# Performance work log

Hardware: AMD Instinct MI355X
Metric: run time of the kernel (lower is better)

## Reference

```python
import jax, jax.numpy as jnp
import numpy as np

B, L, H, R = 4, 192, 768, 24


def setup_inputs() -> dict:
    key = jax.random.key(0)
    ks = jax.random.split(key, 18)
    s = 0.02
    inp = {
        "embed_tokens": jax.random.normal(ks[0], (B, L, H), dtype=jnp.float32),
        "attention_mask": jnp.ones((B, L), dtype=jnp.int32),
        "target_rel": jax.random.randint(ks[1], (B,), 0, R),
        # hidden_relational: Linear(H, H//2) stored as [in, out]
        "W_relh": jax.random.normal(ks[2], (H, H // 2), dtype=jnp.float32) * s,
        "b_relh": jnp.zeros((H // 2,), dtype=jnp.float32),
        # rel_judge: Linear(H//2, R)
        "W_rj": jax.random.normal(ks[3], (H // 2, R), dtype=jnp.float32) * s,
        "b_rj": jnp.zeros((R,), dtype=jnp.float32),
        # hidden_corres: Linear(2H, H)
        "W_corr": jax.random.normal(ks[4], (2 * H, H), dtype=jnp.float32) * s,
        "b_corr": jnp.zeros((H,), dtype=jnp.float32),
        # global_corr: Linear(H, 1)
        "W_gc": jax.random.normal(ks[5], (H, 1), dtype=jnp.float32) * s,
        "b_gc": jnp.zeros((1,), dtype=jnp.float32),
        # rel_embedding: Embedding(R, H)
        "rel_emb": jax.random.normal(ks[6], (R, H), dtype=jnp.float32) * s,
        # hidden_tag: Linear(2H, H) (fusion_type='concat' => multiplier 2)
        "W_tag": jax.random.normal(ks[7], (2 * H, H), dtype=jnp.float32) * s,
        "b_tag": jnp.zeros((H,), dtype=jnp.float32),
        # tag_subject / tag_object: Linear(H, 3)
        "W_sub": jax.random.normal(ks[8], (H, 3), dtype=jnp.float32) * s,
        "b_sub": jnp.zeros((3,), dtype=jnp.float32),
        "W_obj": jax.random.normal(ks[9], (H, 3), dtype=jnp.float32) * s,
        "b_obj": jnp.zeros((3,), dtype=jnp.float32),
    }
    return inp


def reference(embed_tokens, attention_mask, target_rel,
              W_relh, b_relh, W_rj, b_rj,
              W_corr, b_corr, W_gc, b_gc,
              rel_emb, W_tag, b_tag,
              W_sub, b_sub, W_obj, b_obj):
    # mode == 'train' path of PRGC.forward, with embed_tokens standing in for
    # bert(...)['last_hidden_state'].
    mask = attention_mask.astype(embed_tokens.dtype)  # [B,L]
    # stage 1: masked average pool -> relation judgement
    avg = jnp.sum(embed_tokens * mask[:, :, None], axis=1) / jnp.sum(mask, axis=1)[:, None]  # [B,H]
    rel_hidden = jax.nn.relu(avg @ W_relh + b_relh)
    stage1 = rel_hidden @ W_rj + b_rj  # [B,R]

    # correspondence matrix. concat_matrix[b,i,j] = [embed[b,j], embed[b,i]]
    # Linear on a concat is separable: split W_corr into the halves acting on
    # each operand, compute two [B,L,H] projections, sum with broadcasting.
    Hd = W_corr.shape[0] // 2
    h_first = embed_tokens @ W_corr[:Hd]   # acts on embed[b,j]
    h_second = embed_tokens @ W_corr[Hd:]  # acts on embed[b,i]
    corres_hidden = jax.nn.relu(h_first[:, None, :, :] + h_second[:, :, None, :] + b_corr)  # [B,L,L,H]
    pred_corres = corres_hidden @ W_gc + b_gc  # [B,L,L,1]

    # stage 2 tagging (train mode: gather gold relation embeddings)
    rel_e = rel_emb[target_rel]  # [B,H]
    rel_e = jnp.broadcast_to(rel_e[:, None, :], embed_tokens.shape)  # [B,L,H]
    fusion = jnp.concatenate([rel_e, embed_tokens], axis=-1) @ W_tag + b_tag  # [B,L,H] (no activation, as in source)
    subj_pred_tag = fusion @ W_sub + b_sub  # [B,L,3]
    obj_pred_tag = fusion @ W_obj + b_obj   # [B,L,3]
    return (stage1, subj_pred_tag, obj_pred_tag, pred_corres)
```

## Files before the change

kernel.cpp:

```cpp
#include <hip/hip_runtime.h>

#define H   768
#define Hh  384
#define LL  192
#define RR  24
#define HH  589824

typedef __attribute__((ext_vector_type(8))) short bf16x8;
typedef __attribute__((ext_vector_type(4))) float f32x4;

__device__ __forceinline__ unsigned short f2bf(float f) {
    unsigned int u = __float_as_uint(f);
    return (unsigned short)((u + 0x7FFF + ((u >> 16) & 1)) >> 16);
}

__device__ __forceinline__ void gload16(const void* g, void* l) {
    __builtin_amdgcn_global_load_lds(
        (const __attribute__((address_space(1))) unsigned int*)g,
        (__attribute__((address_space(3))) unsigned int*)l, 16, 0, 0);
}

__device__ __forceinline__ float wred(float v) {
#pragma unroll
    for (int off = 1; off < 64; off <<= 1) v += __shfl_xor(v, off);
    return v;
}

__global__ __launch_bounds__(256) void k_pre(
    const float* __restrict__ emb, const int* __restrict__ mask,
    const float* __restrict__ W_corr, const float* __restrict__ W_tag,
    const float* __restrict__ W_gc, const float* __restrict__ b_corr,
    const float* __restrict__ W_sub, const float* __restrict__ b_sub,
    const float* __restrict__ W_obj, const float* __restrict__ b_obj,
    const float* __restrict__ b_tag,
    float* __restrict__ avg_ws, unsigned short* __restrict__ embh,
    unsigned short* __restrict__ wct0, unsigned short* __restrict__ wct1,
    float* __restrict__ W8_ws, float* __restrict__ V8_ws,
    float* __restrict__ cb_ws, float* __restrict__ bc_ws)
{
    const int bid = blockIdx.x, tid = threadIdx.x;

    if (bid < 24) {
        __shared__ float msk[LL];
        __shared__ float part[32];
        __shared__ float msumS;
        __shared__ float4 red4[8][32];
        const int b  = bid / 6;
        const int h0 = (bid % 6) * 128;
        const int tx = tid & 31, ty = tid >> 5;
        if (tid < LL) msk[tid] = (float)mask[b * LL + tid];
        __syncthreads();
        if (tid < 32) {
            float s = 0.f;
            for (int k = tid; k < LL; k += 32) s += msk[k];
            part[tid] = s;
        }
        __syncthreads();
        if (tid == 0) {
            float s = 0.f;
            for (int k = 0; k < 32; ++k) s += part[k];
            msumS = s;
        }
        float4 acc = make_float4(0.f, 0.f, 0.f, 0.f);
        for (int l = ty; l < LL; l += 8) {
            const size_t o = (size_t)(b * LL + l) * H + h0 + tx * 4;
            const float m = msk[l];
            const float4 v = *(const float4*)(emb + o);
            acc.x += v.x * m; acc.y += v.y * m; acc.z += v.z * m; acc.w += v.w * m;
            ushort4 pk;
            pk.x = f2bf(v.x); pk.y = f2bf(v.y); pk.z = f2bf(v.z); pk.w = f2bf(v.w);
            *(ushort4*)(embh + o) = pk;
        }
        red4[ty][tx] = acc;
        __syncthreads();
        if (tid < 32) {
            float4 s = red4[0][tid];
#pragma unroll
            for (int r = 1; r < 8; ++r) {
                s.x += red4[r][tid].x; s.y += red4[r][tid].y;
                s.z += red4[r][tid].z; s.w += red4[r][tid].w;
            }
            const float inv = 1.f / msumS;
            s.x *= inv; s.y *= inv; s.z *= inv; s.w *= inv;
            *(float4*)(avg_ws + (size_t)b * H + h0 + tid * 4) = s;
        }
        return;
    }

    if (bid < 600) {
        const int local = bid - 24;
        const int m  = local / 288;
        const int r2 = local % 288;
        const int ko = r2 / 3, nb = r2 % 3;
        const int n  = nb * 256 + tid;
        const float* src = (m == 0) ? W_corr : W_corr + HH;
        unsigned short* dst = (m == 0) ? wct0 : wct1;
        union { unsigned short u[8]; uint4 v; } pk;
#pragma unroll
        for (int q = 0; q < 8; ++q)
            pk.u[q] = f2bf(src[(size_t)(ko * 8 + q) * H + n]);
        *(uint4*)(dst + (size_t)n * H + ko * 8) = pk.v;
        return;
    }

    if (bid < 792) {
        const int wave = tid >> 6, lane = tid & 63;
        const int k = (bid - 600) * 4 + wave;
        const float* rc0 = W_corr + (size_t)k * H;
        const float* rc1 = W_corr + (size_t)HH + (size_t)k * H;
        const float* rtl = W_tag + (size_t)k * H;
        const float* rth = W_tag + (size_t)(H + k) * H;
        float u0 = 0.f, u1 = 0.f;
        float wsv[3] = {0, 0, 0}, wov[3] = {0, 0, 0};
        float vsv[3] = {0, 0, 0}, vov[3] = {0, 0, 0};
#pragma unroll
        for (int it = 0; it < 3; ++it) {
            const int h = lane * 4 + it * 256;
            const float4 c0 = *(const float4*)(rc0 + h);
            const float4 c1 = *(const float4*)(rc1 + h);
            const float4 tl = *(const float4*)(rtl + h);
            const float4 th = *(const float4*)(rth + h);
            const float4 g  = *(const float4*)(W_gc + h);
            float su[12], ob[12];
            *(float4*)&su[0] = *(const float4*)(W_sub + h * 3);
            *(float4*)&su[4] = *(const float4*)(W_sub + h * 3 + 4);
            *(float4*)&su[8] = *(const float4*)(W_sub + h * 3 + 8);
            *(float4*)&ob[0] = *(const float4*)(W_obj + h * 3);
            *(float4*)&ob[4] = *(const float4*)(W_obj + h * 3 + 4);
            *(float4*)&ob[8] = *(const float4*)(W_obj + h * 3 + 8);
            u0 += c0.x * g.x + c0.y * g.y + c0.z * g.z + c0.w * g.w;
            u1 += c1.x * g.x + c1.y * g.y + c1.z * g.z + c1.w * g.w;
            const float t4[4] = {th.x, th.y, th.z, th.w};
            const float l4[4] = {tl.x, tl.y, tl.z, tl.w};
#pragma unroll
            for (int d = 0; d < 4; ++d)
#pragma unroll
                for (int c = 0; c < 3; ++c) {
                    wsv[c] += t4[d] * su[d * 3 + c];
                    vsv[c] += l4[d] * su[d * 3 + c];
                    wov[c] += t4[d] * ob[d * 3 + c];
                    vov[c] += l4[d] * ob[d * 3 + c];
                }
        }
        u0 = wred(u0); u1 = wred(u1);
#pragma unroll
        for (int c = 0; c < 3; ++c) {
            wsv[c] = wred(wsv[c]); wov[c] = wred(wov[c]);
            vsv[c] = wred(vsv[c]); vov[c] = wred(vov[c]);
        }
        if (lane == 0) {
            *(float4*)(W8_ws + k * 8)     = make_float4(u0, u1, wsv[0], wsv[1]);
            *(float4*)(W8_ws + k * 8 + 4) = make_float4(wsv[2], wov[0], wov[1], wov[2]);
            *(float4*)(V8_ws + k * 8)     = make_float4(vsv[0], vsv[1], vsv[2], vov[0]);
            *(float4*)(V8_ws + k * 8 + 4) = make_float4(vov[1], vov[2], 0.f, 0.f);
        }
        return;
    }

    {
        const int wave = tid >> 6, lane = tid & 63;
        if (wave == 0) {
            float cs[3] = {0, 0, 0}, co[3] = {0, 0, 0};
#pragma unroll
            for (int it = 0; it < 3; ++it) {
                const int h = lane * 4 + it * 256;
                const float4 bt = *(const float4*)(b_tag + h);
                float su[12], ob[12];
                *(float4*)&su[0] = *(const float4*)(W_sub + h * 3);
                *(float4*)&su[4] = *(const float4*)(W_sub + h * 3 + 4);
                *(float4*)&su[8] = *(const float4*)(W_sub + h * 3 + 8);
                *(float4*)&ob[0] = *(const float4*)(W_obj + h * 3);
                *(float4*)&ob[4] = *(const float4*)(W_obj + h * 3 + 4);
                *(float4*)&ob[8] = *(const float4*)(W_obj + h * 3 + 8);
                const float b4[4] = {bt.x, bt.y, bt.z, bt.w};
#pragma unroll
                for (int d = 0; d < 4; ++d)
#pragma unroll
                    for (int c = 0; c < 3; ++c) {
                        cs[c] += b4[d] * su[d * 3 + c];
                        co[c] += b4[d] * ob[d * 3 + c];
                    }
            }
#pragma unroll
            for (int c = 0; c < 3; ++c) { cs[c] = wred(cs[c]); co[c] = wred(co[c]); }
            if (lane == 0) {
#pragma unroll
                for (int c = 0; c < 3; ++c) {
                    cb_ws[c]     = cs[c] + b_sub[c];
                    cb_ws[3 + c] = co[c] + b_obj[c];
                }
            }
        } else if (wave == 1) {
            float s = 0.f;
#pragma unroll
            for (int it = 0; it < 3; ++it) {
                const int h = lane * 4 + it * 256;
                const float4 bcv = *(const float4*)(b_corr + h);
                const float4 g   = *(const float4*)(W_gc + h);
                s += bcv.x * g.x + bcv.y * g.y + bcv.z * g.z + bcv.w * g.w;
            }
            s = wred(s);
            if (lane == 0) bc_ws[0] = s;
        }
    }
}

__global__ __launch_bounds__(256) void k_main(
    const unsigned short* __restrict__ embh, const unsigned short* __restrict__ wct0,
    const unsigned short* __restrict__ wct1, const float* __restrict__ b_corr,
    const float* __restrict__ W_relh, const float* __restrict__ avg_ws,
    const int* __restrict__ target_rel, const float* __restrict__ rel_emb,
    const float* __restrict__ V8_ws, const float* __restrict__ cb_ws,
    float* __restrict__ hfb, float* __restrict__ hsb,
    float* __restrict__ relh_part, float* __restrict__ tb_ws)
{
    __shared__ unsigned short As[2][4096];
    __shared__ unsigned short Bs[2][4096];
    const int bid = blockIdx.x, tid = threadIdx.x;

    if (bid >= 288) {
        if (bid < 480) {
            float* red = (float*)&As[0][0];
            const int rb = bid - 288;
            const int kc = rb & 7;
            const int t2 = rb >> 3;
            const int b  = t2 / 6;
            const int o0 = (t2 % 6) * 64;
            const int tx = tid & 63, ty = tid >> 6;
            const int h0 = kc * 96 + ty * 24;
            float s = 0.f;
            for (int h = h0; h < h0 + 24; ++h)
                s += avg_ws[(size_t)b * H + h] * W_relh[(size_t)h * Hh + o0 + tx];
            red[ty * 64 + tx] = s;
            __syncthreads();
            if (ty == 0)
                relh_part[(size_t)(kc * 4 + b) * Hh + o0 + tx] =
                    red[tx] + red[64 + tx] + red[128 + tx] + red[192 + tx];
        } else {
            const int b = tid >> 6, lane = tid & 63;
            const float* re = rel_emb + (size_t)target_rel[b] * H;
            float t[6] = {0, 0, 0, 0, 0, 0};
#pragma unroll
            for (int it = 0; it < 12; ++it) {
                const int k = lane + it * 64;
                const float rl = re[k];
                const float4 a = *(const float4*)(V8_ws + k * 8);
                const float4 v = *(const float4*)(V8_ws + k * 8 + 4);
                t[0] += rl * a.x; t[1] += rl * a.y; t[2] += rl * a.z;
                t[3] += rl * a.w; t[4] += rl * v.x; t[5] += rl * v.y;
            }
#pragma unroll
            for (int c = 0; c < 6; ++c) t[c] = wred(t[c]);
            if (lane == 0) {
#pragma unroll
                for (int c = 0; c < 6; ++c)
                    tb_ws[b * 8 + c] = t[c] + cb_ws[c];
            }
        }
        return;
    }

    const int sel = bid / 144;
    const int tt  = bid % 144;
    const int mt = tt % 12, nt = tt / 12;
    const int m0 = mt * 64, n0 = nt * 64;
    const unsigned short* Bsrc = sel ? wct1 : wct0;
    float* C = sel ? hsb : hfb;

    const int wv = tid >> 6, ln = tid & 63;
    const int lr = ln & 15, ko = ln >> 4;
    const int wr = (wv >> 1) * 32, wc = (wv & 1) * 32;

    f32x4 acc[2][2];
#pragma unroll
    for (int mi = 0; mi < 2; ++mi)
#pragma unroll
        for (int ni = 0; ni < 2; ++ni)
            acc[mi][ni] = (f32x4){0.f, 0.f, 0.f, 0.f};

    auto stage = [&](int buf, int k0) {
#pragma unroll
        for (int it = 0; it < 2; ++it) {
            const int sbase = it * 256 + wv * 64;
            const int slot = sbase + ln;
            const int r = slot >> 3, c = slot & 7;
            const int cs = c ^ (r & 7);
            gload16(embh + (size_t)(m0 + r) * H + k0 + cs * 8, &As[buf][sbase * 8]);
            gload16(Bsrc + (size_t)(n0 + r) * H + k0 + cs * 8, &Bs[buf][sbase * 8]);
        }
    };

    stage(0, 0);
    int cur = 0;
    for (int ks = 0; ks < 12; ++ks) {
        __syncthreads();
        if (ks < 11) stage(cur ^ 1, (ks + 1) * 64);
        bf16x8 af[2][2], bfr[2][2];
#pragma unroll
        for (int mi = 0; mi < 2; ++mi) {
            const int r = wr + mi * 16 + lr;
#pragma unroll
            for (int kc = 0; kc < 2; ++kc) {
                const int qs = (kc * 4 + ko) ^ (r & 7);
                af[kc][mi] = *(const bf16x8*)(&As[cur][r * 64 + qs * 8]);
            }
        }
#pragma unroll
        for (int ni = 0; ni < 2; ++ni) {
            const int r = wc + ni * 16 + lr;
#pragma unroll
            for (int kc = 0; kc < 2; ++kc) {
                const int qs = (kc * 4 + ko) ^ (r & 7);
                bfr[kc][ni] = *(const bf16x8*)(&Bs[cur][r * 64 + qs * 8]);
            }
        }
#pragma unroll
        for (int kc = 0; kc < 2; ++kc)
#pragma unroll
            for (int mi = 0; mi < 2; ++mi)
#pragma unroll
                for (int ni = 0; ni < 2; ++ni)
                    acc[mi][ni] = __builtin_amdgcn_mfma_f32_16x16x32_bf16(
                        af[kc][mi], bfr[kc][ni], acc[mi][ni], 0, 0, 0);
        cur ^= 1;
    }

    float cbv[2];
#pragma unroll
    for (int ni = 0; ni < 2; ++ni)
        cbv[ni] = (sel == 0) ? b_corr[n0 + wc + ni * 16 + lr] : 0.f;
#pragma unroll
    for (int mi = 0; mi < 2; ++mi)
#pragma unroll
        for (int ni = 0; ni < 2; ++ni) {
            const int m = m0 + wr + mi * 16 + ko * 4;
            const int n = n0 + wc + ni * 16 + lr;
#pragma unroll
            for (int rr = 0; rr < 4; ++rr)
                C[(size_t)(m + rr) * H + n] = acc[mi][ni][rr] + cbv[ni];
        }
}

__global__ __launch_bounds__(256) void k_tail(
    const float* __restrict__ hfb, const float* __restrict__ hsb,
    const float* __restrict__ emb, const float* __restrict__ W8_ws,
    const float* __restrict__ tb_ws, const float* __restrict__ relh_part,
    const float* __restrict__ b_relh, const float* __restrict__ W_gc,
    const float* __restrict__ W_rj, const float* __restrict__ b_rj,
    float* __restrict__ cpart, float* __restrict__ hfw_ws,
    float* __restrict__ out)
{
    __shared__ float hfT[96][34];
    const int bid = blockIdx.x, tid = threadIdx.x;

    if (bid < 576) {
        const int s    = bid & 7;
        const int tile = bid >> 3;
        const int b   = tile / 18;
        const int rem = tile % 18;
        const int i0  = (rem / 6) * 64;
        const int j0  = (rem % 6) * 32;
        const int h0  = s * 96;
        const int tx = tid & 15, ty = tid >> 4;

#pragma unroll
        for (int it = 0; it < 3; ++it) {
            const int j = tid >> 3, q = tid & 7;
            const int k = it * 32 + q * 4;
            const float4 fv = *(const float4*)(hfb + (size_t)(b * LL + j0 + j) * H + h0 + k);
            hfT[k + 0][j] = fv.x;
            hfT[k + 1][j] = fv.y;
            hfT[k + 2][j] = fv.z;
            hfT[k + 3][j] = fv.w;
        }
        __syncthreads();

        float acc[4][2] = {{0.f}};
        float hsr[4][8];
        const float* hsbase = hsb + (size_t)(b * LL + i0 + ty * 4) * H + h0;

        for (int kb = 0; kb < 96; kb += 8) {
#pragma unroll
            for (int ii = 0; ii < 4; ++ii) {
                const float4 v0 = *(const float4*)(hsbase + (size_t)ii * H + kb);
                const float4 v1 = *(const float4*)(hsbase + (size_t)ii * H + kb + 4);
                hsr[ii][0] = v0.x; hsr[ii][1] = v0.y; hsr[ii][2] = v0.z; hsr[ii][3] = v0.w;
                hsr[ii][4] = v1.x; hsr[ii][5] = v1.y; hsr[ii][6] = v1.z; hsr[ii][7] = v1.w;
            }
            const float4 wa = *(const float4*)(W_gc + h0 + kb);
            const float4 wb = *(const float4*)(W_gc + h0 + kb + 4);
            const float wreg[8] = {wa.x, wa.y, wa.z, wa.w, wb.x, wb.y, wb.z, wb.w};
#pragma unroll
            for (int k8 = 0; k8 < 8; ++k8) {
                const int kk = kb + k8;
                const float2 f2 = *(const float2*)&hfT[kk][tx * 2];
                const float w = wreg[k8];
#pragma unroll
                for (int ii = 0; ii < 4; ++ii) {
                    acc[ii][0] += fabsf(f2.x + hsr[ii][k8]) * w;
                    acc[ii][1] += fabsf(f2.y + hsr[ii][k8]) * w;
                }
            }
        }
#pragma unroll
        for (int ii = 0; ii < 4; ++ii) {
            *(float2*)(cpart + (size_t)s * 147456 + (size_t)b * 36864
                       + (size_t)(i0 + ty * 4 + ii) * LL + j0 + tx * 2) =
                make_float2(acc[ii][0], acc[ii][1]);
        }
    } else if (bid < 768) {
        const int wave = tid >> 6, lane = tid & 63;
        const int r = (bid - 576) * 4 + wave;
        const int b = r / LL;
        const float* er = emb + (size_t)r * H;
        float s0 = 0.f, s1 = 0.f;
        float t[6] = {0, 0, 0, 0, 0, 0};
#pragma unroll
        for (int it = 0; it < 12; ++it) {
            const int h = lane + it * 64;
            const float e = er[h];
            const float4 a = *(const float4*)(W8_ws + h * 8);
            const float4 v = *(const float4*)(W8_ws + h * 8 + 4);
            s0 += e * a.x; s1 += e * a.y;
            t[0] += e * a.z; t[1] += e * a.w; t[2] += e * v.x;
            t[3] += e * v.y; t[4] += e * v.z; t[5] += e * v.w;
        }
        s0 = wred(s0); s1 = wred(s1);
#pragma unroll
        for (int c = 0; c < 6; ++c) t[c] = wred(t[c]);
        if (lane == 0) {
            hfw_ws[r] = s0;
            hfw_ws[768 + r] = s1;
#pragma unroll
            for (int c = 0; c < 3; ++c) {
                out[96 + r * 3 + c]   = t[c]     + tb_ws[b * 8 + c];
                out[2400 + r * 3 + c] = t[3 + c] + tb_ws[b * 8 + 3 + c];
            }
        }
    } else {
        float* relhS = &hfT[0][0];
        for (int i = tid; i < 4 * Hh; i += 256) {
            const int b = i / Hh, o = i % Hh;
            float s = b_relh[o];
#pragma unroll
            for (int kc = 0; kc < 8; ++kc)
                s += relh_part[(size_t)(kc * 4 + b) * Hh + o];
            relhS[i] = fmaxf(s, 0.f);
        }
        __syncthreads();
        if (tid < 96) {
            const int b = tid / RR, rj = tid % RR;
            float s = b_rj[rj];
            for (int k = 0; k < Hh; ++k)
                s += relhS[b * Hh + k] * W_rj[k * RR + rj];
            out[b * RR + rj] = s;
        }
    }
}

__global__ __launch_bounds__(256) void k_merge(
    const float* __restrict__ cpart, const float* __restrict__ hfw_ws,
    const float* __restrict__ bc_ws, const float* __restrict__ b_gc,
    float* __restrict__ out)
{
    const int idx = blockIdx.x * 256 + threadIdx.x;
    const int b  = idx / 9216;
    const int rr = idx % 9216;
    const int i  = rr / 48;
    const int j4 = (rr % 48) * 4;
    const size_t off = (size_t)b * 36864 + (size_t)i * LL + j4;

    float4 p = make_float4(0.f, 0.f, 0.f, 0.f);
#pragma unroll
    for (int s = 0; s < 8; ++s) {
        const float4 v = *(const float4*)(cpart + (size_t)s * 147456 + off);
        p.x += v.x; p.y += v.y; p.z += v.z; p.w += v.w;
    }
    const float4 hw = *(const float4*)(hfw_ws + b * LL + j4);
    const float hs = hfw_ws[768 + b * LL + i];
    const float bc = bc_ws[0];
    const float bg = b_gc[0];

    float4 o;
    o.x = 0.5f * (p.x + hw.x + hs + bc) + bg;
    o.y = 0.5f * (p.y + hw.y + hs + bc) + bg;
    o.z = 0.5f * (p.z + hw.z + hs + bc) + bg;
    o.w = 0.5f * (p.w + hw.w + hs + bc) + bg;
    *(float4*)(out + 4704 + off) = o;
}

extern "C" void kernel_launch(void* const* d_in, const int* in_sizes, int n_in,
                              void* d_out, int out_size, void* d_ws, size_t ws_size,
                              hipStream_t stream) {
    const float* emb    = (const float*)d_in[0];
    const int*   mask   = (const int*)d_in[1];
    const int*   trel   = (const int*)d_in[2];
    const float* W_relh = (const float*)d_in[3];
    const float* b_relh = (const float*)d_in[4];
    const float* W_rj   = (const float*)d_in[5];
    const float* b_rj   = (const float*)d_in[6];
    const float* W_corr = (const float*)d_in[7];
    const float* b_corr = (const float*)d_in[8];
    const float* W_gc   = (const float*)d_in[9];
    const float* b_gc   = (const float*)d_in[10];
    const float* relemb = (const float*)d_in[11];
    const float* W_tag  = (const float*)d_in[12];
    const float* b_tag  = (const float*)d_in[13];
    const float* W_sub  = (const float*)d_in[14];
    const float* b_sub  = (const float*)d_in[15];
    const float* W_obj  = (const float*)d_in[16];
    const float* b_obj  = (const float*)d_in[17];

    float* out = (float*)d_out;
    float* ws  = (float*)d_ws;
    float* hfb  = ws;
    float* hsb  = ws + (size_t)HH;
    unsigned short* embh = (unsigned short*)(ws + (size_t)2 * HH);
    unsigned short* wct0 = embh + (size_t)HH;
    unsigned short* wct1 = wct0 + (size_t)HH;
    float* smalls    = ws + (size_t)2 * HH + (size_t)3 * HH / 2;
    float* avg_ws    = smalls;
    float* W8_ws     = avg_ws + 4 * H;
    float* V8_ws     = W8_ws + 8 * H;
    float* relh_part = V8_ws + 8 * H;
    float* hfw_ws    = relh_part + 32 * Hh;
    float* tb_ws     = hfw_ws + 1536;
    float* cb_ws     = tb_ws + 32;
    float* bc_ws     = cb_ws + 8;
    float* cpart     = bc_ws + 8 + 200;

    k_pre<<<793, 256, 0, stream>>>(emb, mask, W_corr, W_tag, W_gc, b_corr,
                                   W_sub, b_sub, W_obj, b_obj, b_tag,
                                   avg_ws, embh, wct0, wct1,
                                   W8_ws, V8_ws, cb_ws, bc_ws);
    k_main<<<481, 256, 0, stream>>>(embh, wct0, wct1, b_corr,
                                    W_relh, avg_ws, trel, relemb,
                                    V8_ws, cb_ws,
                                    hfb, hsb, relh_part, tb_ws);
    k_tail<<<769, 256, 0, stream>>>(hfb, hsb, emb, W8_ws, tb_ws,
                                    relh_part, b_relh, W_gc, W_rj, b_rj,
                                    cpart, hfw_ws, out);
    k_merge<<<144, 256, 0, stream>>>(cpart, hfw_ws, bc_ws, b_gc, out);
}
```

Before: 52.91 us.

## Fuse prep into GEMM kernel, convert fp32 to bf16 on load, merge tail stages

Drops the separate pre-pass that converted embeddings and W_corr to bf16 workspaces. The GEMM blocks now load fp32 operands through registers, convert them to bf16 and write them to LDS with register double-buffering. The masked-average and relation-hidden partials, the weight folding and the bias work become side blocks in the same launch. The tag-bias reduction moves into the second kernel, and the merge, tag output and stage-1 head are combined into a third kernel, going from four launches to three. This removes one launch and the bf16 round trip through global memory, at the cost of fp32 global reads and conversion work inside the GEMM main loop, plus a per-block redundant average recompute.

```diff
diff --git a/kernel.cpp b/kernel.cpp
--- a/kernel.cpp
+++ b/kernel.cpp
@@ -14,157 +14,90 @@
     return (unsigned short)((u + 0x7FFF + ((u >> 16) & 1)) >> 16);
 }
 
-__device__ __forceinline__ void gload16(const void* g, void* l) {
-    __builtin_amdgcn_global_load_lds(
-        (const __attribute__((address_space(1))) unsigned int*)g,
-        (__attribute__((address_space(3))) unsigned int*)l, 16, 0, 0);
-}
-
 __device__ __forceinline__ float wred(float v) {
 #pragma unroll
     for (int off = 1; off < 64; off <<= 1) v += __shfl_xor(v, off);
     return v;
 }
 
-__global__ __launch_bounds__(256) void k_pre(
+__global__ __launch_bounds__(256) void k_A(
     const float* __restrict__ emb, const int* __restrict__ mask,
     const float* __restrict__ W_corr, const float* __restrict__ W_tag,
-    const float* __restrict__ W_gc, const float* __restrict__ b_corr,
+    const float* __restrict__ W_gc, const float* __restrict__ W_relh,
     const float* __restrict__ W_sub, const float* __restrict__ b_sub,
     const float* __restrict__ W_obj, const float* __restrict__ b_obj,
-    const float* __restrict__ b_tag,
-    float* __restrict__ avg_ws, unsigned short* __restrict__ embh,
-    unsigned short* __restrict__ wct0, unsigned short* __restrict__ wct1,
+    const float* __restrict__ b_tag, const float* __restrict__ b_corr,
+    float* __restrict__ hfb, float* __restrict__ hsb,
+    float* __restrict__ relh_part,
     float* __restrict__ W8_ws, float* __restrict__ V8_ws,
     float* __restrict__ cb_ws, float* __restrict__ bc_ws)
 {
+    __shared__ unsigned short As[2][4096];
+    __shared__ unsigned short Bs[2][4096];
     const int bid = blockIdx.x, tid = threadIdx.x;
 
-    if (bid < 24) {
-        __shared__ float msk[LL];
-        __shared__ float part[32];
-        __shared__ float msumS;
-        __shared__ float4 red4[8][32];
-        const int b  = bid / 6;
-        const int h0 = (bid % 6) * 128;
-        const int tx = tid & 31, ty = tid >> 5;
-        if (tid < LL) msk[tid] = (float)mask[b * LL + tid];
-        __syncthreads();
-        if (tid < 32) {
+    if (bid >= 288) {
+        if (bid < 480) {
+            float* sp   = (float*)&As[0][0];
+            float* msk  = sp;
+            float* red2 = sp + 192;
+            float* avgS = sp + 384;
+            float* msum = sp + 480;
+            float* red  = sp + 512;
+            const int rb = bid - 288;
+            const int kc = rb & 7;
+            const int t2 = rb >> 3;
+            const int b  = t2 / 6;
+            const int o0 = (t2 % 6) * 64;
+            if (tid < 192) msk[tid] = (float)mask[b * LL + tid];
+            __syncthreads();
+            if (tid < 64) {
+                float s = msk[tid] + msk[64 + tid] + msk[128 + tid];
+                s = wred(s);
+                if (tid == 0) msum[0] = s;
+            }
+            if (tid < 192) {
+                const int h  = tid % 96;
+                const int lh = tid / 96;
+                float s = 0.f;
+                for (int i = 0; i < 96; ++i) {
+                    const int l = lh * 96 + i;
+                    s += msk[l] * emb[(size_t)(b * LL + l) * H + kc * 96 + h];
+                }
+                red2[lh * 96 + h] = s;
+            }
+            __syncthreads();
+            if (tid < 96)
+                avgS[tid] = (red2[tid] + red2[96 + tid]) / msum[0];
+            __syncthreads();
+            const int tx = tid & 63, ty = tid >> 6;
             float s = 0.f;
-            for (int k = tid; k < LL; k += 32) s += msk[k];
-            part[tid] = s;
-        }
-        __syncthreads();
-        if (tid == 0) {
-            float s = 0.f;
-            for (int k = 0; k < 32; ++k) s += part[k];
-            msumS = s;
-        }
-        float4 acc = make_float4(0.f, 0.f, 0.f, 0.f);
-        for (int l = ty; l < LL; l += 8) {
-            const size_t o = (size_t)(b * LL + l) * H + h0 + tx * 4;
-            const float m = msk[l];
-            const float4 v = *(const float4*)(emb + o);
-            acc.x += v.x * m; acc.y += v.y * m; acc.z += v.z * m; acc.w += v.w * m;
-            ushort4 pk;
-            pk.x = f2bf(v.x); pk.y = f2bf(v.y); pk.z = f2bf(v.z); pk.w = f2bf(v.w);
-            *(ushort4*)(embh + o) = pk;
-        }
-        red4[ty][tx] = acc;
-        __syncthreads();
-        if (tid < 32) {
-            float4 s = red4[0][tid];
-#pragma unroll
-            for (int r = 1; r < 8; ++r) {
-                s.x += red4[r][tid].x; s.y += red4[r][tid].y;
-                s.z += red4[r][tid].z; s.w += red4[r][tid].w;
-            }
-            const float inv = 1.f / msumS;
-            s.x *= inv; s.y *= inv; s.z *= inv; s.w *= inv;
-            *(float4*)(avg_ws + (size_t)b * H + h0 + tid * 4) = s;
-        }
-        return;
-    }
-
-    if (bid < 600) {
-        const int local = bid - 24;
-        const int m  = local / 288;
-        const int r2 = local % 288;
-        const int ko = r2 / 3, nb = r2 % 3;
-        const int n  = nb * 256 + tid;
-        const float* src = (m == 0) ? W_corr : W_corr + HH;
-        unsigned short* dst = (m == 0) ? wct0 : wct1;
-        union { unsigned short u[8]; uint4 v; } pk;
-#pragma unroll
-        for (int q = 0; q < 8; ++q)
-            pk.u[q] = f2bf(src[(size_t)(ko * 8 + q) * H + n]);
-        *(uint4*)(dst + (size_t)n * H + ko * 8) = pk.v;
-        return;
-    }
-
-    if (bid < 792) {
-        const int wave = tid >> 6, lane = tid & 63;
-        const int k = (bid - 600) * 4 + wave;
-        const float* rc0 = W_corr + (size_t)k * H;
-        const float* rc1 = W_corr + (size_t)HH + (size_t)k * H;
-        const float* rtl = W_tag + (size_t)k * H;
-        const float* rth = W_tag + (size_t)(H + k) * H;
-        float u0 = 0.f, u1 = 0.f;
-        float wsv[3] = {0, 0, 0}, wov[3] = {0, 0, 0};
-        float vsv[3] = {0, 0, 0}, vov[3] = {0, 0, 0};
-#pragma unroll
-        for (int it = 0; it < 3; ++it) {
-            const int h = lane * 4 + it * 256;
-            const float4 c0 = *(const float4*)(rc0 + h);
-            const float4 c1 = *(const float4*)(rc1 + h);
-            const float4 tl = *(const float4*)(rtl + h);
-            const float4 th = *(const float4*)(rth + h);
-            const float4 g  = *(const float4*)(W_gc + h);
-            float su[12], ob[12];
-            *(float4*)&su[0] = *(const float4*)(W_sub + h * 3);
-            *(float4*)&su[4] = *(const float4*)(W_sub + h * 3 + 4);
-            *(float4*)&su[8] = *(const float4*)(W_sub + h * 3 + 8);
-            *(float4*)&ob[0] = *(const float4*)(W_obj + h * 3);
-            *(float4*)&ob[4] = *(const float4*)(W_obj + h * 3 + 4);
-            *(float4*)&ob[8] = *(const float4*)(W_obj + h * 3 + 8);
-            u0 += c0.x * g.x + c0.y * g.y + c0.z * g.z + c0.w * g.w;
-            u1 += c1.x * g.x + c1.y * g.y + c1.z * g.z + c1.w * g.w;
-            const float t4[4] = {th.x, th.y, th.z, th.w};
-            const float l4[4] = {tl.x, tl.y, tl.z, tl.w};
-#pragma unroll
-            for (int d = 0; d < 4; ++d)
-#pragma unroll
-                for (int c = 0; c < 3; ++c) {
-                    wsv[c] += t4[d] * su[d * 3 + c];
-                    vsv[c] += l4[d] * su[d * 3 + c];
-                    wov[c] += t4[d] * ob[d * 3 + c];
-                    vov[c] += l4[d] * ob[d * 3 + c];
-                }
-        }
-        u0 = wred(u0); u1 = wred(u1);
-#pragma unroll
-        for (int c = 0; c < 3; ++c) {
-            wsv[c] = wred(wsv[c]); wov[c] = wred(wov[c]);
-            vsv[c] = wred(vsv[c]); vov[c] = wred(vov[c]);
-        }
-        if (lane == 0) {
-            *(float4*)(W8_ws + k * 8)     = make_float4(u0, u1, wsv[0], wsv[1]);
-            *(float4*)(W8_ws + k * 8 + 4) = make_float4(wsv[2], wov[0], wov[1], wov[2]);
-            *(float4*)(V8_ws + k * 8)     = make_float4(vsv[0], vsv[1], vsv[2], vov[0]);
-            *(float4*)(V8_ws + k * 8 + 4) = make_float4(vov[1], vov[2], 0.f, 0.f);
-        }
-        return;
-    }
-
-    {
-        const int wave = tid >> 6, lane = tid & 63;
-        if (wave == 0) {
-            float cs[3] = {0, 0, 0}, co[3] = {0, 0, 0};
+            for (int hh = 0; hh < 24; ++hh)
+                s += avgS[ty * 24 + hh] *
+                     W_relh[(size_t)(kc * 96 + ty * 24 + hh) * Hh + o0 + tx];
+            red[ty * 64 + tx] = s;
+            __syncthreads();
+            if (ty == 0)
+                relh_part[(size_t)(kc * 4 + b) * Hh + o0 + tx] =
+                    red[tx] + red[64 + tx] + red[128 + tx] + red[192 + tx];
+        } else if (bid < 672) {
+            const int wave = tid >> 6, lane = tid & 63;
+            const int k = (bid - 480) * 4 + wave;
+            const float* rc0 = W_corr + (size_t)k * H;
+            const float* rc1 = W_corr + (size_t)HH + (size_t)k * H;
+            const float* rtl = W_tag + (size_t)k * H;
+            const float* rth = W_tag + (size_t)(H + k) * H;
+            float u0 = 0.f, u1 = 0.f;
+            float wsv[3] = {0, 0, 0}, wov[3] = {0, 0, 0};
+            float vsv[3] = {0, 0, 0}, vov[3] = {0, 0, 0};
 #pragma unroll
             for (int it = 0; it < 3; ++it) {
                 const int h = lane * 4 + it * 256;
-                const float4 bt = *(const float4*)(b_tag + h);
+                const float4 c0 = *(const float4*)(rc0 + h);
+                const float4 c1 = *(const float4*)(rc1 + h);
+                const float4 tl = *(const float4*)(rtl + h);
+                const float4 th = *(const float4*)(rth + h);
+                const float4 g  = *(const float4*)(W_gc + h);
                 float su[12], ob[12];
                 *(float4*)&su[0] = *(const float4*)(W_sub + h * 3);
                 *(float4*)&su[4] = *(const float4*)(W_sub + h * 3 + 4);
@@ -172,89 +105,76 @@
                 *(float4*)&ob[0] = *(const float4*)(W_obj + h * 3);
                 *(float4*)&ob[4] = *(const float4*)(W_obj + h * 3 + 4);
                 *(float4*)&ob[8] = *(const float4*)(W_obj + h * 3 + 8);
-                const float b4[4] = {bt.x, bt.y, bt.z, bt.w};
+                u0 += c0.x * g.x + c0.y * g.y + c0.z * g.z + c0.w * g.w;
+                u1 += c1.x * g.x + c1.y * g.y + c1.z * g.z + c1.w * g.w;
+                const float t4[4] = {th.x, th.y, th.z, th.w};
+                const float l4[4] = {tl.x, tl.y, tl.z, tl.w};
 #pragma unroll
                 for (int d = 0; d < 4; ++d)
 #pragma unroll
                     for (int c = 0; c < 3; ++c) {
-                        cs[c] += b4[d] * su[d * 3 + c];
-                        co[c] += b4[d] * ob[d * 3 + c];
+                        wsv[c] += t4[d] * su[d * 3 + c];
+                        vsv[c] += l4[d] * su[d * 3 + c];
+                        wov[c] += t4[d] * ob[d * 3 + c];
+                        vov[c] += l4[d] * ob[d * 3 + c];
                     }
             }
-#pragma unroll
-            for (int c = 0; c < 3; ++c) { cs[c] = wred(cs[c]); co[c] = wred(co[c]); }
+            u0 = wred(u0); u1 = wred(u1);
+#pragma unroll
+            for (int c = 0; c < 3; ++c) {
+                wsv[c] = wred(wsv[c]); wov[c] = wred(wov[c]);
+                vsv[c] = wred(vsv[c]); vov[c] = wred(vov[c]);
+            }
             if (lane == 0) {
-#pragma unroll
-                for (int c = 0; c < 3; ++c) {
-                    cb_ws[c]     = cs[c] + b_sub[c];
-                    cb_ws[3 + c] = co[c] + b_obj[c];
+                *(float4*)(W8_ws + k * 8)     = make_float4(u0, u1, wsv[0], wsv[1]);
+                *(float4*)(W8_ws + k * 8 + 4) = make_float4(wsv[2], wov[0], wov[1], wov[2]);
+                *(float4*)(V8_ws + k * 8)     = make_float4(vsv[0], vsv[1], vsv[2], vov[0]);
+                *(float4*)(V8_ws + k * 8 + 4) = make_float4(vov[1], vov[2], 0.f, 0.f);
+            }
+        } else {
+            const int wave = tid >> 6, lane = tid & 63;
+            if (wave == 0) {
+                float cs[3] = {0, 0, 0}, co[3] = {0, 0, 0};
+#pragma unroll
+                for (int it = 0; it < 3; ++it) {
+                    const int h = lane * 4 + it * 256;
+                    const float4 bt = *(const float4*)(b_tag + h);
+                    float su[12], ob[12];
+                    *(float4*)&su[0] = *(const float4*)(W_sub + h * 3);
+                    *(float4*)&su[4] = *(const float4*)(W_sub + h * 3 + 4);
+                    *(float4*)&su[8] = *(const float4*)(W_sub + h * 3 + 8);
+                    *(float4*)&ob[0] = *(const float4*)(W_obj + h * 3);
+                    *(float4*)&ob[4] = *(const float4*)(W_obj + h * 3 + 4);
+                    *(float4*)&ob[8] = *(const float4*)(W_obj + h * 3 + 8);
+                    const float b4[4] = {bt.x, bt.y, bt.z, bt.w};
+#pragma unroll
+                    for (int d = 0; d < 4; ++d)
+#pragma unroll
+                        for (int c = 0; c < 3; ++c) {
+                            cs[c] += b4[d] * su[d * 3 + c];
+                            co[c] += b4[d] * ob[d * 3 + c];
+                        }
                 }
-            }
-        } else if (wave == 1) {
-            float s = 0.f;
-#pragma unroll
-            for (int it = 0; it < 3; ++it) {
-                const int h = lane * 4 + it * 256;
-                const float4 bcv = *(const float4*)(b_corr + h);
-                const float4 g   = *(const float4*)(W_gc + h);
-                s += bcv.x * g.x + bcv.y * g.y + bcv.z * g.z + bcv.w * g.w;
-            }
-            s = wred(s);
-            if (lane == 0) bc_ws[0] = s;
-        }
-    }
-}
-
-__global__ __launch_bounds__(256) void k_main(
-    const unsigned short* __restrict__ embh, const unsigned short* __restrict__ wct0,
-    const unsigned short* __restrict__ wct1, const float* __restrict__ b_corr,
-    const float* __restrict__ W_relh, const float* __restrict__ avg_ws,
-    const int* __restrict__ target_rel, const float* __restrict__ rel_emb,
-    const float* __restrict__ V8_ws, const float* __restrict__ cb_ws,
-    float* __restrict__ hfb, float* __restrict__ hsb,
-    float* __restrict__ relh_part, float* __restrict__ tb_ws)
-{
-    __shared__ unsigned short As[2][4096];
-    __shared__ unsigned short Bs[2][4096];
-    const int bid = blockIdx.x, tid = threadIdx.x;
-
-    if (bid >= 288) {
-        if (bid < 480) {
-            float* red = (float*)&As[0][0];
-            const int rb = bid - 288;
-            const int kc = rb & 7;
-            const int t2 = rb >> 3;
-            const int b  = t2 / 6;
-            const int o0 = (t2 % 6) * 64;
-            const int tx = tid & 63, ty = tid >> 6;
-            const int h0 = kc * 96 + ty * 24;
-            float s = 0.f;
-            for (int h = h0; h < h0 + 24; ++h)
-                s += avg_ws[(size_t)b * H + h] * W_relh[(size_t)h * Hh + o0 + tx];
-            red[ty * 64 + tx] = s;
-            __syncthreads();
-            if (ty == 0)
-                relh_part[(size_t)(kc * 4 + b) * Hh + o0 + tx] =
-                    red[tx] + red[64 + tx] + red[128 + tx] + red[192 + tx];
-        } else {
-            const int b = tid >> 6, lane = tid & 63;
-            const float* re = rel_emb + (size_t)target_rel[b] * H;
-            float t[6] = {0, 0, 0, 0, 0, 0};
-#pragma unroll
-            for (int it = 0; it < 12; ++it) {
-                const int k = lane + it * 64;
-                const float rl = re[k];
-                const float4 a = *(const float4*)(V8_ws + k * 8);
-                const float4 v = *(const float4*)(V8_ws + k * 8 + 4);
-                t[0] += rl * a.x; t[1] += rl * a.y; t[2] += rl * a.z;
-                t[3] += rl * a.w; t[4] += rl * v.x; t[5] += rl * v.y;
-            }
-#pragma unroll
-            for (int c = 0; c < 6; ++c) t[c] = wred(t[c]);
-            if (lane == 0) {
-#pragma unroll
-                for (int c = 0; c < 6; ++c)
-                    tb_ws[b * 8 + c] = t[c] + cb_ws[c];
+#pragma unroll
+                for (int c = 0; c < 3; ++c) { cs[c] = wred(cs[c]); co[c] = wred(co[c]); }
+                if (lane == 0) {
+#pragma unroll
+                    for (int c = 0; c < 3; ++c) {
+                        cb_ws[c]     = cs[c] + b_sub[c];
+                        cb_ws[3 + c] = co[c] + b_obj[c];
+                    }
+                }
+            } else if (wave == 1) {
+                float s = 0.f;
+#pragma unroll
+                for (int it = 0; it < 3; ++it) {
+                    const int h = lane * 4 + it * 256;
+                    const float4 bcv = *(const float4*)(b_corr + h);
+                    const float4 g   = *(const float4*)(W_gc + h);
+                    s += bcv.x * g.x + bcv.y * g.y + bcv.z * g.z + bcv.w * g.w;
+                }
+                s = wred(s);
+                if (lane == 0) bc_ws[0] = s;
             }
         }
         return;
@@ -264,13 +184,51 @@
     const int tt  = bid % 144;
     const int mt = tt % 12, nt = tt / 12;
     const int m0 = mt * 64, n0 = nt * 64;
-    const unsigned short* Bsrc = sel ? wct1 : wct0;
+    const float* Bsrc = W_corr + (size_t)sel * HH;
     float* C = sel ? hsb : hfb;
 
     const int wv = tid >> 6, ln = tid & 63;
     const int lr = ln & 15, ko = ln >> 4;
     const int wr = (wv >> 1) * 32, wc = (wv & 1) * 32;
 
+    const int am = tid >> 2, akq = tid & 3;
+    const int bk4 = tid >> 4, bn4 = tid & 15;
+
+    float4 ra[4], rb[4];
+    auto loadA = [&](int k0) {
+        const float* src = emb + (size_t)(m0 + am) * H + k0 + akq * 16;
+#pragma unroll
+        for (int q = 0; q < 4; ++q) ra[q] = *(const float4*)(src + q * 4);
+    };
+    auto loadB = [&](int k0) {
+        const float* src = Bsrc + (size_t)(k0 + bk4 * 4) * H + n0 + bn4 * 4;
+#pragma unroll
+        for (int q = 0; q < 4; ++q) rb[q] = *(const float4*)(src + (size_t)q * H);
+    };
+    auto writeAB = [&](int buf) {
+        unsigned short t16[16];
+#pragma unroll
+        for (int q = 0; q < 4; ++q) {
+            t16[q * 4 + 0] = f2bf(ra[q].x); t16[q * 4 + 1] = f2bf(ra[q].y);
+            t16[q * 4 + 2] = f2bf(ra[q].z); t16[q * 4 + 3] = f2bf(ra[q].w);
+        }
+#pragma unroll
+        for (int j = 0; j < 2; ++j)
+            *(uint4*)(&As[buf][am * 64 + (((akq * 2 + j) ^ (am & 7)) * 8)]) =
+                *(uint4*)(&t16[j * 8]);
+#pragma unroll
+        for (int ni = 0; ni < 4; ++ni) {
+            const int n = bn4 * 4 + ni;
+            unsigned long long pk =
+                  (unsigned long long)f2bf((&rb[0].x)[ni])
+                | ((unsigned long long)f2bf((&rb[1].x)[ni]) << 16)
+                | ((unsigned long long)f2bf((&rb[2].x)[ni]) << 32)
+                | ((unsigned long long)f2bf((&rb[3].x)[ni]) << 48);
+            *(unsigned long long*)(&Bs[buf][n * 64 + ((bk4 >> 1) ^ (n & 7)) * 8
+                                            + (bk4 & 1) * 4]) = pk;
+        }
+    };
+
     f32x4 acc[2][2];
 #pragma unroll
     for (int mi = 0; mi < 2; ++mi)
@@ -278,23 +236,16 @@
         for (int ni = 0; ni < 2; ++ni)
             acc[mi][ni] = (f32x4){0.f, 0.f, 0.f, 0.f};
 
-    auto stage = [&](int buf, int k0) {
-#pragma unroll
-        for (int it = 0; it < 2; ++it) {
-            const int sbase = it * 256 + wv * 64;
-            const int slot = sbase + ln;
-            const int r = slot >> 3, c = slot & 7;
-            const int cs = c ^ (r & 7);
-            gload16(embh + (size_t)(m0 + r) * H + k0 + cs * 8, &As[buf][sbase * 8]);
-            gload16(Bsrc + (size_t)(n0 + r) * H + k0 + cs * 8, &Bs[buf][sbase * 8]);
-        }
-    };
-
-    stage(0, 0);
+    loadA(0); loadB(0);
+    writeAB(0);
+    loadA(64); loadB(64);
     int cur = 0;
     for (int ks = 0; ks < 12; ++ks) {
         __syncthreads();
-        if (ks < 11) stage(cur ^ 1, (ks + 1) * 64);
+        if (ks < 11) {
+            writeAB(cur ^ 1);
+            if (ks < 10) { loadA((ks + 2) * 64); loadB((ks + 2) * 64); }
+        }
         bf16x8 af[2][2], bfr[2][2];
 #pragma unroll
         for (int mi = 0; mi < 2; ++mi) {
@@ -341,14 +292,14 @@
         }
 }
 
-__global__ __launch_bounds__(256) void k_tail(
+__global__ __launch_bounds__(256) void k_B(
     const float* __restrict__ hfb, const float* __restrict__ hsb,
     const float* __restrict__ emb, const float* __restrict__ W8_ws,
-    const float* __restrict__ tb_ws, const float* __restrict__ relh_part,
-    const float* __restrict__ b_relh, const float* __restrict__ W_gc,
-    const float* __restrict__ W_rj, const float* __restrict__ b_rj,
+    const float* __restrict__ V8_ws, const float* __restrict__ cb_ws,
+    const int* __restrict__ target_rel, const float* __restrict__ rel_emb,
+    const float* __restrict__ W_gc,
     float* __restrict__ cpart, float* __restrict__ hfw_ws,
-    float* __restrict__ out)
+    float* __restrict__ traw, float* __restrict__ tb_ws)
 {
     __shared__ float hfT[96][34];
     const int bid = blockIdx.x, tid = threadIdx.x;
@@ -411,7 +362,6 @@
     } else if (bid < 768) {
         const int wave = tid >> 6, lane = tid & 63;
         const int r = (bid - 576) * 4 + wave;
-        const int b = r / LL;
         const float* er = emb + (size_t)r * H;
         float s0 = 0.f, s1 = 0.f;
         float t[6] = {0, 0, 0, 0, 0, 0};
@@ -432,61 +382,92 @@
             hfw_ws[r] = s0;
             hfw_ws[768 + r] = s1;
 #pragma unroll
-            for (int c = 0; c < 3; ++c) {
-                out[96 + r * 3 + c]   = t[c]     + tb_ws[b * 8 + c];
-                out[2400 + r * 3 + c] = t[3 + c] + tb_ws[b * 8 + 3 + c];
-            }
+            for (int c = 0; c < 6; ++c) traw[r * 6 + c] = t[c];
         }
     } else {
-        float* relhS = &hfT[0][0];
+        const int b = tid >> 6, lane = tid & 63;
+        const float* re = rel_emb + (size_t)target_rel[b] * H;
+        float t[6] = {0, 0, 0, 0, 0, 0};
+#pragma unroll
+        for (int it = 0; it < 12; ++it) {
+            const int k = lane + it * 64;
+            const float rl = re[k];
+            const float4 a = *(const float4*)(V8_ws + k * 8);
+            const float4 v = *(const float4*)(V8_ws + k * 8 + 4);
+            t[0] += rl * a.x; t[1] += rl * a.y; t[2] += rl * a.z;
+            t[3] += rl * a.w; t[4] += rl * v.x; t[5] += rl * v.y;
+        }
+#pragma unroll
+        for (int c = 0; c < 6; ++c) t[c] = wred(t[c]);
+        if (lane == 0) {
+#pragma unroll
+            for (int c = 0; c < 6; ++c)
+                tb_ws[b * 8 + c] = t[c] + cb_ws[c];
+        }
+    }
+}
+
+__global__ __launch_bounds__(256) void k_C(
+    const float* __restrict__ cpart, const float* __restrict__ hfw_ws,
+    const float* __restrict__ traw, const float* __restrict__ tb_ws,
+    const float* __restrict__ bc_ws, const float* __restrict__ relh_part,
+    const float* __restrict__ b_relh, const float* __restrict__ W_rj,
+    const float* __restrict__ b_rj, const float* __restrict__ b_gc,
+    float* __restrict__ out)
+{
+    __shared__ float pool[1536];
+    const int bid = blockIdx.x, tid = threadIdx.x;
+
+    if (bid < 144) {
+        const int idx = bid * 256 + tid;
+        const int b  = idx / 9216;
+        const int rr = idx % 9216;
+        const int i  = rr / 48;
+        const int j4 = (rr % 48) * 4;
+        const size_t off = (size_t)b * 36864 + (size_t)i * LL + j4;
+
+        float4 p = make_float4(0.f, 0.f, 0.f, 0.f);
+#pragma unroll
+        for (int s = 0; s < 8; ++s) {
+            const float4 v = *(const float4*)(cpart + (size_t)s * 147456 + off);
+            p.x += v.x; p.y += v.y; p.z += v.z; p.w += v.w;
+        }
+        const float4 hw = *(const float4*)(hfw_ws + b * LL + j4);
+        const float hs = hfw_ws[768 + b * LL + i];
+        const float bc = bc_ws[0];
+        const float bg = b_gc[0];
+
+        float4 o;
+        o.x = 0.5f * (p.x + hw.x + hs + bc) + bg;
+        o.y = 0.5f * (p.y + hw.y + hs + bc) + bg;
+        o.z = 0.5f * (p.z + hw.z + hs + bc) + bg;
+        o.w = 0.5f * (p.w + hw.w + hs + bc) + bg;
+        *(float4*)(out + 4704 + off) = o;
+    } else if (bid < 162) {
+        const int idx = (bid - 144) * 256 + tid;
+        const int r = idx / 6, c = idx % 6;
+        const int b = r / LL;
+        const float v = traw[r * 6 + c] + tb_ws[b * 8 + c];
+        if (c < 3) out[96 + r * 3 + c] = v;
+        else       out[2400 + r * 3 + (c - 3)] = v;
+    } else {
         for (int i = tid; i < 4 * Hh; i += 256) {
             const int b = i / Hh, o = i % Hh;
             float s = b_relh[o];
 #pragma unroll
             for (int kc = 0; kc < 8; ++kc)
                 s += relh_part[(size_t)(kc * 4 + b) * Hh + o];
-            relhS[i] = fmaxf(s, 0.f);
+            pool[i] = fmaxf(s, 0.f);
         }
         __syncthreads();
         if (tid < 96) {
             const int b = tid / RR, rj = tid % RR;
             float s = b_rj[rj];
             for (int k = 0; k < Hh; ++k)
-                s += relhS[b * Hh + k] * W_rj[k * RR + rj];
+                s += pool[b * Hh + k] * W_rj[k * RR + rj];
             out[b * RR + rj] = s;
         }
     }
-}
-
-__global__ __launch_bounds__(256) void k_merge(
-    const float* __restrict__ cpart, const float* __restrict__ hfw_ws,
-    const float* __restrict__ bc_ws, const float* __restrict__ b_gc,
-    float* __restrict__ out)
-{
-    const int idx = blockIdx.x * 256 + threadIdx.x;
-    const int b  = idx / 9216;
-    const int rr = idx % 9216;
-    const int i  = rr / 48;
-    const int j4 = (rr % 48) * 4;
-    const size_t off = (size_t)b * 36864 + (size_t)i * LL + j4;
-
-    float4 p = make_float4(0.f, 0.f, 0.f, 0.f);
-#pragma unroll
-    for (int s = 0; s < 8; ++s) {
-        const float4 v = *(const float4*)(cpart + (size_t)s * 147456 + off);
-        p.x += v.x; p.y += v.y; p.z += v.z; p.w += v.w;
-    }
-    const float4 hw = *(const float4*)(hfw_ws + b * LL + j4);
-    const float hs = hfw_ws[768 + b * LL + i];
-    const float bc = bc_ws[0];
-    const float bg = b_gc[0];
-
-    float4 o;
-    o.x = 0.5f * (p.x + hw.x + hs + bc) + bg;
-    o.y = 0.5f * (p.y + hw.y + hs + bc) + bg;
-    o.z = 0.5f * (p.z + hw.z + hs + bc) + bg;
-    o.w = 0.5f * (p.w + hw.w + hs + bc) + bg;
-    *(float4*)(out + 4704 + off) = o;
 }
 
 extern "C" void kernel_launch(void* const* d_in, const int* in_sizes, int n_in,
@@ -515,30 +496,22 @@
     float* ws  = (float*)d_ws;
     float* hfb  = ws;
     float* hsb  = ws + (size_t)HH;
-    unsigned short* embh = (unsigned short*)(ws + (size_t)2 * HH);
-    unsigned short* wct0 = embh + (size_t)HH;
-    unsigned short* wct1 = wct0 + (size_t)HH;
-    float* smalls    = ws + (size_t)2 * HH + (size_t)3 * HH / 2;
-    float* avg_ws    = smalls;
-    float* W8_ws     = avg_ws + 4 * H;
+    float* W8_ws     = ws + (size_t)2 * HH;
     float* V8_ws     = W8_ws + 8 * H;
     float* relh_part = V8_ws + 8 * H;
     float* hfw_ws    = relh_part + 32 * Hh;
-    float* tb_ws     = hfw_ws + 1536;
+    float* traw      = hfw_ws + 1536;
+    float* tb_ws     = traw + 4608;
     float* cb_ws     = tb_ws + 32;
     float* bc_ws     = cb_ws + 8;
-    float* cpart     = bc_ws + 8 + 200;
-
-    k_pre<<<793, 256, 0, stream>>>(emb, mask, W_corr, W_tag, W_gc, b_corr,
-                                   W_sub, b_sub, W_obj, b_obj, b_tag,
-                                   avg_ws, embh, wct0, wct1,
-                                   W8_ws, V8_ws, cb_ws, bc_ws);
-    k_main<<<481, 256, 0, stream>>>(embh, wct0, wct1, b_corr,
-                                    W_relh, avg_ws, trel, relemb,
-                                    V8_ws, cb_ws,
-                                    hfb, hsb, relh_part, tb_ws);
-    k_tail<<<769, 256, 0, stream>>>(hfb, hsb, emb, W8_ws, tb_ws,
-                                    relh_part, b_relh, W_gc, W_rj, b_rj,
-                                    cpart, hfw_ws, out);
-    k_merge<<<144, 256, 0, stream>>>(cpart, hfw_ws, bc_ws, b_gc, out);
+    float* cpart     = bc_ws + 8 + 120;
+
+    k_A<<<673, 256, 0, stream>>>(emb, mask, W_corr, W_tag, W_gc, W_relh,
+                                 W_sub, b_sub, W_obj, b_obj, b_tag, b_corr,
+                                 hfb, hsb, relh_part, W8_ws, V8_ws, cb_ws, bc_ws);
+    k_B<<<769, 256, 0, stream>>>(hfb, hsb, emb, W8_ws, V8_ws, cb_ws,
+                                 trel, relemb, W_gc,
+                                 cpart, hfw_ws, traw, tb_ws);
+    k_C<<<163, 256, 0, stream>>>(cpart, hfw_ws, traw, tb_ws, bc_ws,
+                                 relh_part, b_relh, W_rj, b_rj, b_gc, out);
 }
```

New measurement: 50.82 us. 1.04x faster.
